# Performance work log

Hardware: AMD Instinct MI355X
Metric: run time of the kernel (lower is better)

## Reference

```python
import jax, jax.numpy as jnp
import numpy as np

N = 100000   # nodes
E = 3200000  # edges (avg degree 32)
G = 512      # graphs in batch
IN = 128     # in_channels
H1, C1 = 8, 8  # conv1 heads, per-head channels
OUT = 64     # out_channels (conv2, 1 head)
NEG_SLOPE = 0.2


def setup_inputs() -> dict:
    key = jax.random.key(0)
    ks = jax.random.split(key, 12)
    s = 0.1
    return dict(
        x=jax.random.normal(ks[0], (N, IN), jnp.float32),
        edge_index=jax.random.randint(ks[1], (2, E), 0, N),
        batch=jnp.sort(jax.random.randint(ks[2], (N,), 0, G)),
        W1=jax.random.normal(ks[3], (IN, H1 * C1), jnp.float32) * s,
        att_src1=jax.random.normal(ks[4], (H1, C1), jnp.float32) * s,
        att_dst1=jax.random.normal(ks[5], (H1, C1), jnp.float32) * s,
        b1=jnp.zeros((H1 * C1,), jnp.float32),
        W2=jax.random.normal(ks[6], (H1 * C1, OUT), jnp.float32) * s,
        att_src2=jax.random.normal(ks[7], (1, OUT), jnp.float32) * s,
        att_dst2=jax.random.normal(ks[8], (1, OUT), jnp.float32) * s,
        b2=jnp.zeros((OUT,), jnp.float32),
        lw1=jax.random.normal(ks[9], (OUT, 128), jnp.float32) * s,
        lb1=jnp.zeros((128,), jnp.float32),
        lw2=jax.random.normal(ks[10], (128, 1), jnp.float32) * s,
        lb2=jnp.zeros((1,), jnp.float32),
    )


def gat_layer(x, src, dst, W, a_src, a_dst, bias, heads, outc):
    # PyG GATConv (eval mode): linear -> per-edge leaky_relu attention ->
    # segment softmax over incoming edges per dst -> weighted scatter-add.
    n = x.shape[0]
    h = (x @ W).reshape(n, heads, outc)                      # [N,H,C]
    a_s = jnp.einsum('nhc,hc->nh', h, a_src)                 # [N,H]
    a_d = jnp.einsum('nhc,hc->nh', h, a_dst)
    e = jax.nn.leaky_relu(a_s[src] + a_d[dst], NEG_SLOPE)    # [E',H]
    m = jax.ops.segment_max(e, dst, num_segments=n)
    m = jax.lax.stop_gradient(jnp.where(jnp.isfinite(m), m, 0.0))
    ex = jnp.exp(e - m[dst])
    denom = jax.ops.segment_sum(ex, dst, num_segments=n)
    alpha = ex / jnp.maximum(denom[dst], 1e-16)              # [E',H]
    out = jax.ops.segment_sum(h[src] * alpha[:, :, None], dst, num_segments=n)
    return out.reshape(n, heads * outc) + bias


def reference(x, W1, att_src1, att_dst1, b1, W2, att_src2, att_dst2, b2,
              lw1, lb1, lw2, lb2, edge_index, batch):
    n = x.shape[0]
    loops = jnp.arange(n)                                    # add_self_loops=True
    src = jnp.concatenate([edge_index[0], loops])
    dst = jnp.concatenate([edge_index[1], loops])
    h = jax.nn.elu(gat_layer(x, src, dst, W1, att_src1, att_dst1, b1, H1, C1))
    h = gat_layer(h, src, dst, W2, att_src2, att_dst2, b2, 1, OUT)  # [N,OUT]
    # global_mean_pool
    s = jax.ops.segment_sum(h, batch, num_segments=G)
    cnt = jax.ops.segment_sum(jnp.ones((n, 1), h.dtype), batch, num_segments=G)
    g = s / jnp.maximum(cnt, 1.0)                            # [G,OUT]
    g = jax.nn.elu(g @ lw1 + lb1)
    return g @ lw2 + lb2                                     # [G,1]
```

## Files before the change

### kernel.cpp

```cpp
#include <hip/hip_runtime.h>
#include <hip/hip_fp16.h>
#include <math.h>

#define NN   100000
#define EE   3200000
#define GG   512
#define INC  128
#define D1   64
#define OUTC 64
#define HID  128
#define NEG  0.2f

#define BINS 391
#define BCAP 9216
#define BKBLK 1563
#define NGB 391

typedef __attribute__((ext_vector_type(2))) float v2f;

__global__ __launch_bounds__(256, 3)
void k_fused(const int* __restrict__ srcv, const int* __restrict__ dstv,
             int* __restrict__ cursor, int* __restrict__ bucket,
             const float* __restrict__ x, const float* __restrict__ W1,
             const float* __restrict__ att_s, const float* __restrict__ att_d,
             unsigned int* __restrict__ h1, __half* __restrict__ a_s,
             float* __restrict__ a_d) {
    __shared__ __align__(16) char smem[49152];
    int tid = threadIdx.x;
    if (blockIdx.x < NGB) {
        float4* sW4 = (float4*)smem;
        float (*sxT)[256] = (float(*)[256])(smem + 32768);
        const float4* W4 = (const float4*)W1;
        for (int i = tid; i < 128 * 16; i += 256) sW4[i] = W4[i];
        int node0 = blockIdx.x * 256;
        int rg = tid >> 3, cg = tid & 7;
        float acc[8][8];
#pragma unroll
        for (int ii = 0; ii < 8; ++ii)
#pragma unroll
            for (int jj = 0; jj < 8; ++jj) acc[ii][jj] = 0.f;
        const float4* x4 = (const float4*)x;
        for (int kt = 0; kt < 8; ++kt) {
            if (kt) __syncthreads();
#pragma unroll
            for (int q = 0; q < 4; ++q) {
                int i = q * 256 + tid;
                int r = i >> 2, kc = i & 3;
                int gn = node0 + r;
                float4 v = {0.f, 0.f, 0.f, 0.f};
                if (gn < NN) v = x4[(size_t)gn * 32 + kt * 4 + kc];
                int cs = r ^ (kc << 3);
                sxT[kc * 4 + 0][cs] = v.x;
                sxT[kc * 4 + 1][cs] = v.y;
                sxT[kc * 4 + 2][cs] = v.z;
                sxT[kc * 4 + 3][cs] = v.w;
            }
            __syncthreads();
#pragma unroll 4
            for (int kk = 0; kk < 16; ++kk) {
                int sw = (kk >> 2) << 3;
                const float* xr = &sxT[kk][(rg * 8) ^ sw];
                float4 xa = *(const float4*)xr;
                float4 xb = *(const float4*)(xr + 4);
                int kg = kt * 16 + kk;
                float4 wa = sW4[kg * 16 + cg * 2];
                float4 wb = sW4[kg * 16 + cg * 2 + 1];
                float xv[8] = {xa.x, xa.y, xa.z, xa.w, xb.x, xb.y, xb.z, xb.w};
                float wv[8] = {wa.x, wa.y, wa.z, wa.w, wb.x, wb.y, wb.z, wb.w};
#pragma unroll
                for (int ii = 0; ii < 8; ++ii)
#pragma unroll
                    for (int jj = 0; jj < 8; ++jj)
                        acc[ii][jj] = fmaf(xv[ii], wv[jj], acc[ii][jj]);
            }
        }
        float4 s0 = ((const float4*)att_s)[cg * 2];
        float4 s1 = ((const float4*)att_s)[cg * 2 + 1];
        float4 d0 = ((const float4*)att_d)[cg * 2];
        float4 d1 = ((const float4*)att_d)[cg * 2 + 1];
        uint2* hp2 = (uint2*)h1;
#pragma unroll
        for (int ii = 0; ii < 8; ++ii) {
            int n = node0 + rg * 8 + ii;
            if (n < NN) {
                float* a = acc[ii];
                int p0 = __builtin_amdgcn_cvt_pk_fp8_f32(a[0], a[1], 0, false);
                p0 = __builtin_amdgcn_cvt_pk_fp8_f32(a[2], a[3], p0, true);
                int p1 = __builtin_amdgcn_cvt_pk_fp8_f32(a[4], a[5], 0, false);
                p1 = __builtin_amdgcn_cvt_pk_fp8_f32(a[6], a[7], p1, true);
                uint2 pk; pk.x = (unsigned)p0; pk.y = (unsigned)p1;
                hp2[n * 8 + cg] = pk;
                float as = a[0] * s0.x;
                as = fmaf(a[1], s0.y, as); as = fmaf(a[2], s0.z, as);
                as = fmaf(a[3], s0.w, as); as = fmaf(a[4], s1.x, as);
                as = fmaf(a[5], s1.y, as); as = fmaf(a[6], s1.z, as);
                as = fmaf(a[7], s1.w, as);
                float ad = a[0] * d0.x;
                ad = fmaf(a[1], d0.y, ad); ad = fmaf(a[2], d0.z, ad);
                ad = fmaf(a[3], d0.w, ad); ad = fmaf(a[4], d1.x, ad);
                ad = fmaf(a[5], d1.y, ad); ad = fmaf(a[6], d1.z, ad);
                ad = fmaf(a[7], d1.w, ad);
                a_s[n * 8 + cg] = __float2half(as);
                a_d[n * 8 + cg] = ad;
            }
        }
    } else {
        int* hcnt  = (int*)smem;
        int* hbase = hcnt + BINS;
        for (int i = tid; i < BINS; i += 256) hcnt[i] = 0;
        __syncthreads();
        int e0 = (blockIdx.x - NGB) * 2048;
        int bn[8], rk[8], pk[8];
#pragma unroll
        for (int q = 0; q < 8; ++q) {
            int e = e0 + q * 256 + tid;
            if (e < EE) {
                int s = srcv[e], d = dstv[e];
                bn[q] = d >> 8;
                pk[q] = (s << 8) | (d & 255);
                rk[q] = atomicAdd(&hcnt[bn[q]], 1);
            } else bn[q] = -1;
        }
        __syncthreads();
        for (int i = tid; i < BINS; i += 256) {
            int c = hcnt[i];
            hbase[i] = c ? atomicAdd(&cursor[i], c) : 0;
        }
        __syncthreads();
#pragma unroll
        for (int q = 0; q < 8; ++q) {
            if (bn[q] >= 0) {
                int p = hbase[bn[q]] + rk[q];
                if (p < BCAP) bucket[bn[q] * BCAP + p] = pk[q];
            }
        }
    }
}

__global__ __launch_bounds__(256)
void k_binCSR(const int* __restrict__ cursor, const int* __restrict__ bucket,
              int* __restrict__ col, int* __restrict__ rbeg, int* __restrict__ rend) {
    __shared__ int cnt[256];
    __shared__ int tmp[256];
    __shared__ int cur[256];
    int b = blockIdx.x, tid = threadIdx.x;
    cnt[tid] = 0;
    __syncthreads();
    int m = cursor[b]; if (m > BCAP) m = BCAP;
    const int* seg = bucket + b * BCAP;
    for (int i = tid; i < m; i += 256)
        atomicAdd(&cnt[seg[i] & 255], 1);
    __syncthreads();
    tmp[tid] = cnt[tid];
    __syncthreads();
    for (int off = 1; off < 256; off <<= 1) {
        int t = (tid >= off) ? tmp[tid - off] : 0;
        __syncthreads();
        tmp[tid] += t;
        __syncthreads();
    }
    int excl = tmp[tid] - cnt[tid];
    int n = b * 256 + tid;
    if (n < NN) {
        rbeg[n] = b * BCAP + excl;
        rend[n] = b * BCAP + excl + cnt[tid];
    }
    cur[tid] = excl;
    __syncthreads();
    for (int i = tid; i < m; i += 256) {
        int pkv = seg[i];
        int r = atomicAdd(&cur[pkv & 255], 1);
        col[b * BCAP + r] = pkv >> 8;
    }
}

__global__ __launch_bounds__(256, 8)
void k_gat_agg1(const int* __restrict__ rbeg, const int* __restrict__ rend,
                const int* __restrict__ col,
                const __half* __restrict__ a_s, const float* __restrict__ a_d,
                const unsigned int* __restrict__ h1, const float* __restrict__ b1,
                float* __restrict__ out) {
    int wv = threadIdx.x >> 6;
    int lane = threadIdx.x & 63;
    int half = lane >> 5;
    int d = blockIdx.x * 8 + wv * 2 + half;
    int gs = (lane >> 3) & 3;
    int l = lane & 7;
    int rb = rbeg[d], re = rend[d];
    float adh = a_d[d * 8 + l];
    const uint2* hp = (const uint2*)h1;
    uint2 rself = hp[d * 8 + l];
    float asself = __half2float(a_s[d * 8 + l]);
    float ac[8] = {0.f,0.f,0.f,0.f,0.f,0.f,0.f,0.f};
    float denom = 0.f;
    int e = rb + gs;
    int s[4];
#pragma unroll
    for (int q = 0; q < 4; ++q) s[q] = col[e + 4 * q];
    for (; e + 12 < re; ) {
        uint2 rr[4]; float asv[4]; int sn[4];
#pragma unroll
        for (int q = 0; q < 4; ++q) rr[q] = hp[s[q] * 8 + l];
#pragma unroll
        for (int q = 0; q < 4; ++q) asv[q] = __half2float(a_s[s[q] * 8 + l]);
        int en = e + 16;
#pragma unroll
        for (int q = 0; q < 4; ++q) sn[q] = col[en + 4 * q];
#pragma unroll
        for (int q = 0; q < 4; ++q) {
            float xx = asv[q] + adh;
            xx = xx >= 0.f ? xx : NEG * xx;
            float w = __expf(xx);
            denom += w;
            v2f f0 = __builtin_amdgcn_cvt_pk_f32_fp8((int)rr[q].x, false);
            v2f f1 = __builtin_amdgcn_cvt_pk_f32_fp8((int)rr[q].x, true);
            v2f f2 = __builtin_amdgcn_cvt_pk_f32_fp8((int)rr[q].y, false);
            v2f f3 = __builtin_amdgcn_cvt_pk_f32_fp8((int)rr[q].y, true);
            ac[0] = fmaf(f0.x, w, ac[0]); ac[1] = fmaf(f0.y, w, ac[1]);
            ac[2] = fmaf(f1.x, w, ac[2]); ac[3] = fmaf(f1.y, w, ac[3]);
            ac[4] = fmaf(f2.x, w, ac[4]); ac[5] = fmaf(f2.y, w, ac[5]);
            ac[6] = fmaf(f3.x, w, ac[6]); ac[7] = fmaf(f3.y, w, ac[7]);
        }
        e = en;
#pragma unroll
        for (int q = 0; q < 4; ++q) s[q] = sn[q];
    }
    for (; e < re; e += 4) {
        int s0 = col[e];
        uint2 r0 = hp[s0 * 8 + l];
        float x0 = __half2float(a_s[s0 * 8 + l]) + adh;
        x0 = x0 >= 0.f ? x0 : NEG * x0;
        float w0 = __expf(x0);
        denom += w0;
        v2f f0 = __builtin_amdgcn_cvt_pk_f32_fp8((int)r0.x, false);
        v2f f1 = __builtin_amdgcn_cvt_pk_f32_fp8((int)r0.x, true);
        v2f f2 = __builtin_amdgcn_cvt_pk_f32_fp8((int)r0.y, false);
        v2f f3 = __builtin_amdgcn_cvt_pk_f32_fp8((int)r0.y, true);
        ac[0] = fmaf(f0.x, w0, ac[0]); ac[1] = fmaf(f0.y, w0, ac[1]);
        ac[2] = fmaf(f1.x, w0, ac[2]); ac[3] = fmaf(f1.y, w0, ac[3]);
        ac[4] = fmaf(f2.x, w0, ac[4]); ac[5] = fmaf(f2.y, w0, ac[5]);
        ac[6] = fmaf(f3.x, w0, ac[6]); ac[7] = fmaf(f3.y, w0, ac[7]);
    }
    if (gs == 0) {
        float es = asself + adh;
        es = es >= 0.f ? es : NEG * es;
        float w = __expf(es);
        denom += w;
        v2f f0 = __builtin_amdgcn_cvt_pk_f32_fp8((int)rself.x, false);
        v2f f1 = __builtin_amdgcn_cvt_pk_f32_fp8((int)rself.x, true);
        v2f f2 = __builtin_amdgcn_cvt_pk_f32_fp8((int)rself.y, false);
        v2f f3 = __builtin_amdgcn_cvt_pk_f32_fp8((int)rself.y, true);
        ac[0] = fmaf(f0.x, w, ac[0]); ac[1] = fmaf(f0.y, w, ac[1]);
        ac[2] = fmaf(f1.x, w, ac[2]); ac[3] = fmaf(f1.y, w, ac[3]);
        ac[4] = fmaf(f2.x, w, ac[4]); ac[5] = fmaf(f2.y, w, ac[5]);
        ac[6] = fmaf(f3.x, w, ac[6]); ac[7] = fmaf(f3.y, w, ac[7]);
    }
#pragma unroll
    for (int i = 0; i < 8; ++i) {
        ac[i] += __shfl_xor(ac[i], 8, 64);
        ac[i] += __shfl_xor(ac[i], 16, 64);
    }
    denom += __shfl_xor(denom, 8, 64);
    denom += __shfl_xor(denom, 16, 64);
    if (gs == 0) {
        float inv = 1.0f / denom;
        float4 b0 = ((const float4*)b1)[l * 2];
        float4 b4 = ((const float4*)b1)[l * 2 + 1];
        float4 r0, r1;
        r0.x = fmaf(ac[0], inv, b0.x); r0.x = r0.x > 0.f ? r0.x : expm1f(r0.x);
        r0.y = fmaf(ac[1], inv, b0.y); r0.y = r0.y > 0.f ? r0.y : expm1f(r0.y);
        r0.z = fmaf(ac[2], inv, b0.z); r0.z = r0.z > 0.f ? r0.z : expm1f(r0.z);
        r0.w = fmaf(ac[3], inv, b0.w); r0.w = r0.w > 0.f ? r0.w : expm1f(r0.w);
        r1.x = fmaf(ac[4], inv, b4.x); r1.x = r1.x > 0.f ? r1.x : expm1f(r1.x);
        r1.y = fmaf(ac[5], inv, b4.y); r1.y = r1.y > 0.f ? r1.y : expm1f(r1.y);
        r1.z = fmaf(ac[6], inv, b4.z); r1.z = r1.z > 0.f ? r1.z : expm1f(r1.z);
        r1.w = fmaf(ac[7], inv, b4.w); r1.w = r1.w > 0.f ? r1.w : expm1f(r1.w);
        ((float4*)out)[d * 16 + l * 2]     = r0;
        ((float4*)out)[d * 16 + l * 2 + 1] = r1;
    }
}

__global__ __launch_bounds__(256, 3)
void k_lin2(const float* __restrict__ hin, const float* __restrict__ W2,
            const float* __restrict__ att_s, const float* __restrict__ att_d,
            unsigned int* __restrict__ h2, float* __restrict__ a_s,
            float* __restrict__ a_d) {
    __shared__ float4 sW4[D1 * 16];
    __shared__ float sxT[32][256];
    int tid = threadIdx.x;
    const float4* W4 = (const float4*)W2;
    for (int i = tid; i < D1 * 16; i += 256) sW4[i] = W4[i];
    int node0 = blockIdx.x * 256;
    int rg = tid >> 3, cg = tid & 7;
    float acc[8][8];
#pragma unroll
    for (int ii = 0; ii < 8; ++ii)
#pragma unroll
        for (int jj = 0; jj < 8; ++jj) acc[ii][jj] = 0.f;
    const float4* x4 = (const float4*)hin;
    for (int kt = 0; kt < 2; ++kt) {
        if (kt) __syncthreads();
#pragma unroll
        for (int q = 0; q < 8; ++q) {
            int i = q * 256 + tid;
            int r = i >> 3, kc = i & 7;
            int gn = node0 + r;
            float4 v = {0.f, 0.f, 0.f, 0.f};
            if (gn < NN) v = x4[(size_t)gn * 16 + kt * 8 + kc];
            int cs = r ^ (kc << 3);
            sxT[kc * 4 + 0][cs] = v.x;
            sxT[kc * 4 + 1][cs] = v.y;
            sxT[kc * 4 + 2][cs] = v.z;
            sxT[kc * 4 + 3][cs] = v.w;
        }
        __syncthreads();
#pragma unroll 4
        for (int kk = 0; kk < 32; ++kk) {
            int sw = (kk >> 2) << 3;
            const float* xr = &sxT[kk][(rg * 8) ^ sw];
            float4 xa = *(const float4*)xr;
            float4 xb = *(const float4*)(xr + 4);
            int kg = kt * 32 + kk;
            float4 wa = sW4[kg * 16 + cg * 2];
            float4 wb = sW4[kg * 16 + cg * 2 + 1];
            float xv[8] = {xa.x, xa.y, xa.z, xa.w, xb.x, xb.y, xb.z, xb.w};
            float wv[8] = {wa.x, wa.y, wa.z, wa.w, wb.x, wb.y, wb.z, wb.w};
#pragma unroll
            for (int ii = 0; ii < 8; ++ii)
#pragma unroll
                for (int jj = 0; jj < 8; ++jj)
                    acc[ii][jj] = fmaf(xv[ii], wv[jj], acc[ii][jj]);
        }
    }
    float4 s0 = ((const float4*)att_s)[cg * 2];
    float4 s1 = ((const float4*)att_s)[cg * 2 + 1];
    float4 d0 = ((const float4*)att_d)[cg * 2];
    float4 d1 = ((const float4*)att_d)[cg * 2 + 1];
    uint2* hp2 = (uint2*)h2;
#pragma unroll
    for (int ii = 0; ii < 8; ++ii) {
        int n = node0 + rg * 8 + ii;
        if (n < NN) {
            float* a = acc[ii];
            int p0 = __builtin_amdgcn_cvt_pk_fp8_f32(a[0], a[1], 0, false);
            p0 = __builtin_amdgcn_cvt_pk_fp8_f32(a[2], a[3], p0, true);
            int p1 = __builtin_amdgcn_cvt_pk_fp8_f32(a[4], a[5], 0, false);
            p1 = __builtin_amdgcn_cvt_pk_fp8_f32(a[6], a[7], p1, true);
            uint2 pk; pk.x = (unsigned)p0; pk.y = (unsigned)p1;
            hp2[n * 8 + cg] = pk;
            float vs = a[0] * s0.x;
            vs = fmaf(a[1], s0.y, vs); vs = fmaf(a[2], s0.z, vs);
            vs = fmaf(a[3], s0.w, vs); vs = fmaf(a[4], s1.x, vs);
            vs = fmaf(a[5], s1.y, vs); vs = fmaf(a[6], s1.z, vs);
            vs = fmaf(a[7], s1.w, vs);
            float vd = a[0] * d0.x;
            vd = fmaf(a[1], d0.y, vd); vd = fmaf(a[2], d0.z, vd);
            vd = fmaf(a[3], d0.w, vd); vd = fmaf(a[4], d1.x, vd);
            vd = fmaf(a[5], d1.y, vd); vd = fmaf(a[6], d1.z, vd);
            vd = fmaf(a[7], d1.w, vd);
            vs += __shfl_xor(vs, 1, 64); vs += __shfl_xor(vs, 2, 64);
            vs += __shfl_xor(vs, 4, 64);
            vd += __shfl_xor(vd, 1, 64); vd += __shfl_xor(vd, 2, 64);
            vd += __shfl_xor(vd, 4, 64);
            if (cg == 0) { a_s[n] = vs; a_d[n] = vd; }
        }
    }
}

__global__ __launch_bounds__(256, 8)
void k_gat_agg2(const int* __restrict__ rbeg, const int* __restrict__ rend,
                const int* __restrict__ col,
                const float* __restrict__ a_s, const float* __restrict__ a_d,
                const unsigned int* __restrict__ h2, const float* __restrict__ b2,
                const int* __restrict__ batch,
                float* __restrict__ pool, float* __restrict__ cnt) {
    __shared__ float sv[8][64];
    __shared__ int sgi[8];
    int wv = threadIdx.x >> 6;
    int lane = threadIdx.x & 63;
    int half = lane >> 5;
    int idx = wv * 2 + half;
    int d = blockIdx.x * 8 + idx;
    int gs = (lane >> 3) & 3;
    int l = lane & 7;
    int rb = rbeg[d], re = rend[d];
    float ad = a_d[d];
    const uint2* hp = (const uint2*)h2;
    uint2 rself = hp[d * 8 + l];
    float asself = a_s[d];
    if (gs == 0 && l == 0) sgi[idx] = batch[d];
    float ac[8] = {0.f,0.f,0.f,0.f,0.f,0.f,0.f,0.f};
    float denom = 0.f;
    int e = rb + gs;
    int s[4];
#pragma unroll
    for (int q = 0; q < 4; ++q) s[q] = col[e + 4 * q];
    for (; e + 12 < re; ) {
        uint2 rr[4]; float asv[4]; int sn[4];
#pragma unroll
        for (int q = 0; q < 4; ++q) rr[q] = hp[s[q] * 8 + l];
#pragma unroll
        for (int q = 0; q < 4; ++q) asv[q] = a_s[s[q]];
        int en = e + 16;
#pragma unroll
        for (int q = 0; q < 4; ++q) sn[q] = col[en + 4 * q];
#pragma unroll
        for (int q = 0; q < 4; ++q) {
            float xx = asv[q] + ad;
            xx = xx >= 0.f ? xx : NEG * xx;
            float w = __expf(xx);
            denom += w;
            v2f f0 = __builtin_amdgcn_cvt_pk_f32_fp8((int)rr[q].x, false);
            v2f f1 = __builtin_amdgcn_cvt_pk_f32_fp8((int)rr[q].x, true);
            v2f f2 = __builtin_amdgcn_cvt_pk_f32_fp8((int)rr[q].y, false);
            v2f f3 = __builtin_amdgcn_cvt_pk_f32_fp8((int)rr[q].y, true);
            ac[0] = fmaf(f0.x, w, ac[0]); ac[1] = fmaf(f0.y, w, ac[1]);
            ac[2] = fmaf(f1.x, w, ac[2]); ac[3] = fmaf(f1.y, w, ac[3]);
            ac[4] = fmaf(f2.x, w, ac[4]); ac[5] = fmaf(f2.y, w, ac[5]);
            ac[6] = fmaf(f3.x, w, ac[6]); ac[7] = fmaf(f3.y, w, ac[7]);
        }
        e = en;
#pragma unroll
        for (int q = 0; q < 4; ++q) s[q] = sn[q];
    }
    for (; e < re; e += 4) {
        int s0 = col[e];
        uint2 r0 = hp[s0 * 8 + l];
        float x0 = a_s[s0] + ad;
        x0 = x0 >= 0.f ? x0 : NEG * x0;
        float w0 = __expf(x0);
        denom += w0;
        v2f f0 = __builtin_amdgcn_cvt_pk_f32_fp8((int)r0.x, false);
        v2f f1 = __builtin_amdgcn_cvt_pk_f32_fp8((int)r0.x, true);
        v2f f2 = __builtin_amdgcn_cvt_pk_f32_fp8((int)r0.y, false);
        v2f f3 = __builtin_amdgcn_cvt_pk_f32_fp8((int)r0.y, true);
        ac[0] = fmaf(f0.x, w0, ac[0]); ac[1] = fmaf(f0.y, w0, ac[1]);
        ac[2] = fmaf(f1.x, w0, ac[2]); ac[3] = fmaf(f1.y, w0, ac[3]);
        ac[4] = fmaf(f2.x, w0, ac[4]); ac[5] = fmaf(f2.y, w0, ac[5]);
        ac[6] = fmaf(f3.x, w0, ac[6]); ac[7] = fmaf(f3.y, w0, ac[7]);
    }
    if (gs == 0) {
        float es = asself + ad;
        es = es >= 0.f ? es : NEG * es;
        float w = __expf(es);
        denom += w;
        v2f f0 = __builtin_amdgcn_cvt_pk_f32_fp8((int)rself.x, false);
        v2f f1 = __builtin_amdgcn_cvt_pk_f32_fp8((int)rself.x, true);
        v2f f2 = __builtin_amdgcn_cvt_pk_f32_fp8((int)rself.y, false);
        v2f f3 = __builtin_amdgcn_cvt_pk_f32_fp8((int)rself.y, true);
        ac[0] = fmaf(f0.x, w, ac[0]); ac[1] = fmaf(f0.y, w, ac[1]);
        ac[2] = fmaf(f1.x, w, ac[2]); ac[3] = fmaf(f1.y, w, ac[3]);
        ac[4] = fmaf(f2.x, w, ac[4]); ac[5] = fmaf(f2.y, w, ac[5]);
        ac[6] = fmaf(f3.x, w, ac[6]); ac[7] = fmaf(f3.y, w, ac[7]);
    }
#pragma unroll
    for (int i = 0; i < 8; ++i) {
        ac[i] += __shfl_xor(ac[i], 8, 64);
        ac[i] += __shfl_xor(ac[i], 16, 64);
    }
    denom += __shfl_xor(denom, 8, 64);
    denom += __shfl_xor(denom, 16, 64);
    if (gs == 0) {
        float inv = 1.0f / denom;
#pragma unroll
        for (int i = 0; i < 8; ++i)
            sv[idx][l * 8 + i] = fmaf(ac[i], inv, b2[l * 8 + i]);
    }
    __syncthreads();
    int tid = threadIdx.x;
    if (tid < 64) {
        float acc = sv[0][tid]; int curg = sgi[0];
        for (int r = 1; r < 8; ++r) {
            if (sgi[r] == curg) acc += sv[r][tid];
            else { atomicAdd(&pool[curg * 64 + tid], acc); curg = sgi[r]; acc = sv[r][tid]; }
        }
        atomicAdd(&pool[curg * 64 + tid], acc);
    } else if (tid == 64) {
        float c = 1.f; int curg = sgi[0];
        for (int r = 1; r < 8; ++r) {
            if (sgi[r] == curg) c += 1.f;
            else { atomicAdd(&cnt[curg], c); curg = sgi[r]; c = 1.f; }
        }
        atomicAdd(&cnt[curg], c);
    }
}

__global__ __launch_bounds__(128)
void k_mlp(const float* __restrict__ pool, const float* __restrict__ cnt,
           const float* __restrict__ lw1, const float* __restrict__ lb1,
           const float* __restrict__ lw2, const float* __restrict__ lb2,
           float* __restrict__ out) {
    __shared__ float sg[OUTC];
    __shared__ float sh[HID];
    int g = blockIdx.x, tid = threadIdx.x;
    float c = fmaxf(cnt[g], 1.0f);
    if (tid < OUTC) sg[tid] = pool[g * OUTC + tid] / c;
    __syncthreads();
    float acc = lb1[tid];
#pragma unroll 8
    for (int k = 0; k < OUTC; ++k)
        acc = fmaf(sg[k], lw1[k * HID + tid], acc);
    acc = acc > 0.f ? acc : expm1f(acc);
    sh[tid] = acc * lw2[tid];
    __syncthreads();
    for (int off = 64; off >= 1; off >>= 1) {
        if (tid < off) sh[tid] += sh[tid + off];
        __syncthreads();
    }
    if (tid == 0) out[g] = sh[0] + lb2[0];
}

extern "C" void kernel_launch(void* const* d_in, const int* in_sizes, int n_in,
                              void* d_out, int out_size, void* d_ws, size_t ws_size,
                              hipStream_t stream) {
    const float* x    = (const float*)d_in[0];
    const int*   ei   = (const int*)d_in[1];
    const int*   batch= (const int*)d_in[2];
    const float* W1   = (const float*)d_in[3];
    const float* as1  = (const float*)d_in[4];
    const float* ad1  = (const float*)d_in[5];
    const float* b1   = (const float*)d_in[6];
    const float* W2   = (const float*)d_in[7];
    const float* as2  = (const float*)d_in[8];
    const float* ad2  = (const float*)d_in[9];
    const float* b2   = (const float*)d_in[10];
    const float* lw1  = (const float*)d_in[11];
    const float* lb1  = (const float*)d_in[12];
    const float* lw2  = (const float*)d_in[13];
    const float* lb2  = (const float*)d_in[14];
    float* out = (float*)d_out;

    unsigned int* H8 = (unsigned int*)d_ws;
    float* B    = (float*)(H8 + (size_t)NN * 16);
    float* aD1  = B + (size_t)NN * 64;
    float* aS2  = aD1 + NN * 8;
    float* aD2  = aS2 + NN;
    float* pool = aD2 + NN;
    float* cnt  = pool + GG * 64;
    __half* aS1h = (__half*)(cnt + GG);
    int* rbeg   = (int*)(aS1h + (size_t)NN * 8);
    int* rend   = rbeg + NN;
    int* cursor = rend + NN;
    int* bucket = cursor + BINS;
    int* colv   = bucket + (size_t)BINS * BCAP;

    const int* srcv = ei;
    const int* dstv = ei + EE;

    hipMemsetAsync(cursor, 0, BINS * sizeof(int), stream);
    hipMemsetAsync(pool, 0, (size_t)(GG * 64 + GG) * sizeof(float), stream);

    k_fused<<<NGB + BKBLK, 256, 0, stream>>>(srcv, dstv, cursor, bucket,
                                             x, W1, as1, ad1, H8, aS1h, aD1);
    k_binCSR<<<BINS, 256, 0, stream>>>(cursor, bucket, colv, rbeg, rend);

    k_gat_agg1<<<NN / 8, 256, 0, stream>>>(rbeg, rend, colv, aS1h, aD1, H8, b1, B);

    k_lin2    <<<NGB, 256, 0, stream>>>(B, W2, as2, ad2, H8, aS2, aD2);
    k_gat_agg2<<<NN / 8, 256, 0, stream>>>(rbeg, rend, colv, aS2, aD2, H8, b2, batch, pool, cnt);

    k_mlp<<<GG, 128, 0, stream>>>(pool, cnt, lw1, lb1, lw2, lb2, out);
}
```

Before: 353.2 us.

## Split fp8 feature table into two column slabs and aggregate in two passes

Stores the fp8 node features as two separate half-width slabs (32 channels each) and runs each GAT aggregation kernel twice, once per slab. Each pass gathers only 4 bytes per lane, so a pass's working set of gathered rows is half as large and fits better in cache. The cost is reading the CSR column list, recomputing the attention exponentials twice, and extra launches. Column-index loads and layer-1 output stores are also made nontemporal.

```diff
diff --git a/kernel.cpp b/kernel.cpp
--- a/kernel.cpp
+++ b/kernel.cpp
@@ -17,6 +17,7 @@
 #define NGB 391
 
 typedef __attribute__((ext_vector_type(2))) float v2f;
+typedef __attribute__((ext_vector_type(4))) float v4f;
 
 __global__ __launch_bounds__(256, 3)
 void k_fused(const int* __restrict__ srcv, const int* __restrict__ dstv,
@@ -78,7 +79,8 @@
         float4 s1 = ((const float4*)att_s)[cg * 2 + 1];
         float4 d0 = ((const float4*)att_d)[cg * 2];
         float4 d1 = ((const float4*)att_d)[cg * 2 + 1];
-        uint2* hp2 = (uint2*)h1;
+        uint2* slab2 = (uint2*)(h1 + (size_t)(cg >> 2) * NN * 8);
+        int cj = cg & 3;
 #pragma unroll
         for (int ii = 0; ii < 8; ++ii) {
             int n = node0 + rg * 8 + ii;
@@ -89,7 +91,7 @@
                 int p1 = __builtin_amdgcn_cvt_pk_fp8_f32(a[4], a[5], 0, false);
                 p1 = __builtin_amdgcn_cvt_pk_fp8_f32(a[6], a[7], p1, true);
                 uint2 pk; pk.x = (unsigned)p0; pk.y = (unsigned)p1;
-                hp2[n * 8 + cg] = pk;
+                slab2[n * 4 + cj] = pk;
                 float as = a[0] * s0.x;
                 as = fmaf(a[1], s0.y, as); as = fmaf(a[2], s0.z, as);
                 as = fmaf(a[3], s0.w, as); as = fmaf(a[4], s1.x, as);
@@ -174,6 +176,7 @@
     }
 }
 
+template<int PASS>
 __global__ __launch_bounds__(256, 8)
 void k_gat_agg1(const int* __restrict__ rbeg, const int* __restrict__ rend,
                 const int* __restrict__ col,
@@ -186,77 +189,66 @@
     int d = blockIdx.x * 8 + wv * 2 + half;
     int gs = (lane >> 3) & 3;
     int l = lane & 7;
+    int hd = PASS * 4 + (l >> 1);
+    const unsigned int* hp = h1 + (size_t)PASS * NN * 8;
     int rb = rbeg[d], re = rend[d];
-    float adh = a_d[d * 8 + l];
-    const uint2* hp = (const uint2*)h1;
-    uint2 rself = hp[d * 8 + l];
-    float asself = __half2float(a_s[d * 8 + l]);
-    float ac[8] = {0.f,0.f,0.f,0.f,0.f,0.f,0.f,0.f};
+    float adh = a_d[d * 8 + hd];
+    unsigned int rself = hp[d * 8 + l];
+    float asself = __half2float(a_s[d * 8 + hd]);
+    float ac[4] = {0.f, 0.f, 0.f, 0.f};
     float denom = 0.f;
     int e = rb + gs;
     int s[4];
 #pragma unroll
-    for (int q = 0; q < 4; ++q) s[q] = col[e + 4 * q];
+    for (int q = 0; q < 4; ++q) s[q] = __builtin_nontemporal_load(col + e + 4 * q);
     for (; e + 12 < re; ) {
-        uint2 rr[4]; float asv[4]; int sn[4];
+        unsigned int rr[4]; float asv[4]; int sn[4];
 #pragma unroll
         for (int q = 0; q < 4; ++q) rr[q] = hp[s[q] * 8 + l];
 #pragma unroll
-        for (int q = 0; q < 4; ++q) asv[q] = __half2float(a_s[s[q] * 8 + l]);
+        for (int q = 0; q < 4; ++q) asv[q] = __half2float(a_s[s[q] * 8 + hd]);
         int en = e + 16;
 #pragma unroll
-        for (int q = 0; q < 4; ++q) sn[q] = col[en + 4 * q];
+        for (int q = 0; q < 4; ++q) sn[q] = __builtin_nontemporal_load(col + en + 4 * q);
 #pragma unroll
         for (int q = 0; q < 4; ++q) {
             float xx = asv[q] + adh;
             xx = xx >= 0.f ? xx : NEG * xx;
             float w = __expf(xx);
             denom += w;
-            v2f f0 = __builtin_amdgcn_cvt_pk_f32_fp8((int)rr[q].x, false);
-            v2f f1 = __builtin_amdgcn_cvt_pk_f32_fp8((int)rr[q].x, true);
-            v2f f2 = __builtin_amdgcn_cvt_pk_f32_fp8((int)rr[q].y, false);
-            v2f f3 = __builtin_amdgcn_cvt_pk_f32_fp8((int)rr[q].y, true);
+            v2f f0 = __builtin_amdgcn_cvt_pk_f32_fp8((int)rr[q], false);
+            v2f f1 = __builtin_amdgcn_cvt_pk_f32_fp8((int)rr[q], true);
             ac[0] = fmaf(f0.x, w, ac[0]); ac[1] = fmaf(f0.y, w, ac[1]);
             ac[2] = fmaf(f1.x, w, ac[2]); ac[3] = fmaf(f1.y, w, ac[3]);
-            ac[4] = fmaf(f2.x, w, ac[4]); ac[5] = fmaf(f2.y, w, ac[5]);
-            ac[6] = fmaf(f3.x, w, ac[6]); ac[7] = fmaf(f3.y, w, ac[7]);
         }
         e = en;
 #pragma unroll
         for (int q = 0; q < 4; ++q) s[q] = sn[q];
     }
     for (; e < re; e += 4) {
-        int s0 = col[e];
-        uint2 r0 = hp[s0 * 8 + l];
-        float x0 = __half2float(a_s[s0 * 8 + l]) + adh;
+        int s0 = __builtin_nontemporal_load(col + e);
+        unsigned int r0 = hp[s0 * 8 + l];
+        float x0 = __half2float(a_s[s0 * 8 + hd]) + adh;
         x0 = x0 >= 0.f ? x0 : NEG * x0;
         float w0 = __expf(x0);
         denom += w0;
-        v2f f0 = __builtin_amdgcn_cvt_pk_f32_fp8((int)r0.x, false);
-        v2f f1 = __builtin_amdgcn_cvt_pk_f32_fp8((int)r0.x, true);
-        v2f f2 = __builtin_amdgcn_cvt_pk_f32_fp8((int)r0.y, false);
-        v2f f3 = __builtin_amdgcn_cvt_pk_f32_fp8((int)r0.y, true);
+        v2f f0 = __builtin_amdgcn_cvt_pk_f32_fp8((int)r0, false);
+        v2f f1 = __builtin_amdgcn_cvt_pk_f32_fp8((int)r0, true);
         ac[0] = fmaf(f0.x, w0, ac[0]); ac[1] = fmaf(f0.y, w0, ac[1]);
         ac[2] = fmaf(f1.x, w0, ac[2]); ac[3] = fmaf(f1.y, w0, ac[3]);
-        ac[4] = fmaf(f2.x, w0, ac[4]); ac[5] = fmaf(f2.y, w0, ac[5]);
-        ac[6] = fmaf(f3.x, w0, ac[6]); ac[7] = fmaf(f3.y, w0, ac[7]);
     }
     if (gs == 0) {
         float es = asself + adh;
         es = es >= 0.f ? es : NEG * es;
         float w = __expf(es);
         denom += w;
-        v2f f0 = __builtin_amdgcn_cvt_pk_f32_fp8((int)rself.x, false);
-        v2f f1 = __builtin_amdgcn_cvt_pk_f32_fp8((int)rself.x, true);
-        v2f f2 = __builtin_amdgcn_cvt_pk_f32_fp8((int)rself.y, false);
-        v2f f3 = __builtin_amdgcn_cvt_pk_f32_fp8((int)rself.y, true);
+        v2f f0 = __builtin_amdgcn_cvt_pk_f32_fp8((int)rself, false);
+        v2f f1 = __builtin_amdgcn_cvt_pk_f32_fp8((int)rself, true);
         ac[0] = fmaf(f0.x, w, ac[0]); ac[1] = fmaf(f0.y, w, ac[1]);
         ac[2] = fmaf(f1.x, w, ac[2]); ac[3] = fmaf(f1.y, w, ac[3]);
-        ac[4] = fmaf(f2.x, w, ac[4]); ac[5] = fmaf(f2.y, w, ac[5]);
-        ac[6] = fmaf(f3.x, w, ac[6]); ac[7] = fmaf(f3.y, w, ac[7]);
-    }
-#pragma unroll
-    for (int i = 0; i < 8; ++i) {
+    }
+#pragma unroll
+    for (int i = 0; i < 4; ++i) {
         ac[i] += __shfl_xor(ac[i], 8, 64);
         ac[i] += __shfl_xor(ac[i], 16, 64);
     }
@@ -264,19 +256,13 @@
     denom += __shfl_xor(denom, 16, 64);
     if (gs == 0) {
         float inv = 1.0f / denom;
-        float4 b0 = ((const float4*)b1)[l * 2];
-        float4 b4 = ((const float4*)b1)[l * 2 + 1];
-        float4 r0, r1;
+        float4 b0 = ((const float4*)b1)[PASS * 8 + l];
+        v4f r0;
         r0.x = fmaf(ac[0], inv, b0.x); r0.x = r0.x > 0.f ? r0.x : expm1f(r0.x);
         r0.y = fmaf(ac[1], inv, b0.y); r0.y = r0.y > 0.f ? r0.y : expm1f(r0.y);
         r0.z = fmaf(ac[2], inv, b0.z); r0.z = r0.z > 0.f ? r0.z : expm1f(r0.z);
         r0.w = fmaf(ac[3], inv, b0.w); r0.w = r0.w > 0.f ? r0.w : expm1f(r0.w);
-        r1.x = fmaf(ac[4], inv, b4.x); r1.x = r1.x > 0.f ? r1.x : expm1f(r1.x);
-        r1.y = fmaf(ac[5], inv, b4.y); r1.y = r1.y > 0.f ? r1.y : expm1f(r1.y);
-        r1.z = fmaf(ac[6], inv, b4.z); r1.z = r1.z > 0.f ? r1.z : expm1f(r1.z);
-        r1.w = fmaf(ac[7], inv, b4.w); r1.w = r1.w > 0.f ? r1.w : expm1f(r1.w);
-        ((float4*)out)[d * 16 + l * 2]     = r0;
-        ((float4*)out)[d * 16 + l * 2 + 1] = r1;
+        __builtin_nontemporal_store(r0, (v4f*)out + d * 16 + PASS * 8 + l);
     }
 }
 
@@ -336,7 +322,8 @@
     float4 s1 = ((const float4*)att_s)[cg * 2 + 1];
     float4 d0 = ((const float4*)att_d)[cg * 2];
     float4 d1 = ((const float4*)att_d)[cg * 2 + 1];
-    uint2* hp2 = (uint2*)h2;
+    uint2* slab2 = (uint2*)(h2 + (size_t)(cg >> 2) * NN * 8);
+    int cj = cg & 3;
 #pragma unroll
     for (int ii = 0; ii < 8; ++ii) {
         int n = node0 + rg * 8 + ii;
@@ -347,7 +334,7 @@
             int p1 = __builtin_amdgcn_cvt_pk_fp8_f32(a[4], a[5], 0, false);
             p1 = __builtin_amdgcn_cvt_pk_fp8_f32(a[6], a[7], p1, true);
             uint2 pk; pk.x = (unsigned)p0; pk.y = (unsigned)p1;
-            hp2[n * 8 + cg] = pk;
+            slab2[n * 4 + cj] = pk;
             float vs = a[0] * s0.x;
             vs = fmaf(a[1], s0.y, vs); vs = fmaf(a[2], s0.z, vs);
             vs = fmaf(a[3], s0.w, vs); vs = fmaf(a[4], s1.x, vs);
@@ -367,6 +354,7 @@
     }
 }
 
+template<int PASS>
 __global__ __launch_bounds__(256, 8)
 void k_gat_agg2(const int* __restrict__ rbeg, const int* __restrict__ rend,
                 const int* __restrict__ col,
@@ -374,7 +362,7 @@
                 const unsigned int* __restrict__ h2, const float* __restrict__ b2,
                 const int* __restrict__ batch,
                 float* __restrict__ pool, float* __restrict__ cnt) {
-    __shared__ float sv[8][64];
+    __shared__ float sv[8][32];
     __shared__ int sgi[8];
     int wv = threadIdx.x >> 6;
     int lane = threadIdx.x & 63;
@@ -383,78 +371,66 @@
     int d = blockIdx.x * 8 + idx;
     int gs = (lane >> 3) & 3;
     int l = lane & 7;
+    const unsigned int* hp = h2 + (size_t)PASS * NN * 8;
     int rb = rbeg[d], re = rend[d];
     float ad = a_d[d];
-    const uint2* hp = (const uint2*)h2;
-    uint2 rself = hp[d * 8 + l];
+    unsigned int rself = hp[d * 8 + l];
     float asself = a_s[d];
     if (gs == 0 && l == 0) sgi[idx] = batch[d];
-    float ac[8] = {0.f,0.f,0.f,0.f,0.f,0.f,0.f,0.f};
+    float ac[4] = {0.f, 0.f, 0.f, 0.f};
     float denom = 0.f;
     int e = rb + gs;
     int s[4];
 #pragma unroll
-    for (int q = 0; q < 4; ++q) s[q] = col[e + 4 * q];
+    for (int q = 0; q < 4; ++q) s[q] = __builtin_nontemporal_load(col + e + 4 * q);
     for (; e + 12 < re; ) {
-        uint2 rr[4]; float asv[4]; int sn[4];
+        unsigned int rr[4]; float asv[4]; int sn[4];
 #pragma unroll
         for (int q = 0; q < 4; ++q) rr[q] = hp[s[q] * 8 + l];
 #pragma unroll
         for (int q = 0; q < 4; ++q) asv[q] = a_s[s[q]];
         int en = e + 16;
 #pragma unroll
-        for (int q = 0; q < 4; ++q) sn[q] = col[en + 4 * q];
+        for (int q = 0; q < 4; ++q) sn[q] = __builtin_nontemporal_load(col + en + 4 * q);
 #pragma unroll
         for (int q = 0; q < 4; ++q) {
             float xx = asv[q] + ad;
             xx = xx >= 0.f ? xx : NEG * xx;
             float w = __expf(xx);
             denom += w;
-            v2f f0 = __builtin_amdgcn_cvt_pk_f32_fp8((int)rr[q].x, false);
-            v2f f1 = __builtin_amdgcn_cvt_pk_f32_fp8((int)rr[q].x, true);
-            v2f f2 = __builtin_amdgcn_cvt_pk_f32_fp8((int)rr[q].y, false);
-            v2f f3 = __builtin_amdgcn_cvt_pk_f32_fp8((int)rr[q].y, true);
+            v2f f0 = __builtin_amdgcn_cvt_pk_f32_fp8((int)rr[q], false);
+            v2f f1 = __builtin_amdgcn_cvt_pk_f32_fp8((int)rr[q], true);
             ac[0] = fmaf(f0.x, w, ac[0]); ac[1] = fmaf(f0.y, w, ac[1]);
             ac[2] = fmaf(f1.x, w, ac[2]); ac[3] = fmaf(f1.y, w, ac[3]);
-            ac[4] = fmaf(f2.x, w, ac[4]); ac[5] = fmaf(f2.y, w, ac[5]);
-            ac[6] = fmaf(f3.x, w, ac[6]); ac[7] = fmaf(f3.y, w, ac[7]);
         }
         e = en;
 #pragma unroll
         for (int q = 0; q < 4; ++q) s[q] = sn[q];
     }
     for (; e < re; e += 4) {
-        int s0 = col[e];
-        uint2 r0 = hp[s0 * 8 + l];
+        int s0 = __builtin_nontemporal_load(col + e);
+        unsigned int r0 = hp[s0 * 8 + l];
         float x0 = a_s[s0] + ad;
         x0 = x0 >= 0.f ? x0 : NEG * x0;
         float w0 = __expf(x0);
         denom += w0;
-        v2f f0 = __builtin_amdgcn_cvt_pk_f32_fp8((int)r0.x, false);
-        v2f f1 = __builtin_amdgcn_cvt_pk_f32_fp8((int)r0.x, true);
-        v2f f2 = __builtin_amdgcn_cvt_pk_f32_fp8((int)r0.y, false);
-        v2f f3 = __builtin_amdgcn_cvt_pk_f32_fp8((int)r0.y, true);
+        v2f f0 = __builtin_amdgcn_cvt_pk_f32_fp8((int)r0, false);
+        v2f f1 = __builtin_amdgcn_cvt_pk_f32_fp8((int)r0, true);
         ac[0] = fmaf(f0.x, w0, ac[0]); ac[1] = fmaf(f0.y, w0, ac[1]);
         ac[2] = fmaf(f1.x, w0, ac[2]); ac[3] = fmaf(f1.y, w0, ac[3]);
-        ac[4] = fmaf(f2.x, w0, ac[4]); ac[5] = fmaf(f2.y, w0, ac[5]);
-        ac[6] = fmaf(f3.x, w0, ac[6]); ac[7] = fmaf(f3.y, w0, ac[7]);
     }
     if (gs == 0) {
         float es = asself + ad;
         es = es >= 0.f ? es : NEG * es;
         float w = __expf(es);
         denom += w;
-        v2f f0 = __builtin_amdgcn_cvt_pk_f32_fp8((int)rself.x, false);
-        v2f f1 = __builtin_amdgcn_cvt_pk_f32_fp8((int)rself.x, true);
-        v2f f2 = __builtin_amdgcn_cvt_pk_f32_fp8((int)rself.y, false);
-        v2f f3 = __builtin_amdgcn_cvt_pk_f32_fp8((int)rself.y, true);
+        v2f f0 = __builtin_amdgcn_cvt_pk_f32_fp8((int)rself, false);
+        v2f f1 = __builtin_amdgcn_cvt_pk_f32_fp8((int)rself, true);
         ac[0] = fmaf(f0.x, w, ac[0]); ac[1] = fmaf(f0.y, w, ac[1]);
         ac[2] = fmaf(f1.x, w, ac[2]); ac[3] = fmaf(f1.y, w, ac[3]);
-        ac[4] = fmaf(f2.x, w, ac[4]); ac[5] = fmaf(f2.y, w, ac[5]);
-        ac[6] = fmaf(f3.x, w, ac[6]); ac[7] = fmaf(f3.y, w, ac[7]);
-    }
-#pragma unroll
-    for (int i = 0; i < 8; ++i) {
+    }
+#pragma unroll
+    for (int i = 0; i < 4; ++i) {
         ac[i] += __shfl_xor(ac[i], 8, 64);
         ac[i] += __shfl_xor(ac[i], 16, 64);
     }
@@ -463,19 +439,19 @@
     if (gs == 0) {
         float inv = 1.0f / denom;
 #pragma unroll
-        for (int i = 0; i < 8; ++i)
-            sv[idx][l * 8 + i] = fmaf(ac[i], inv, b2[l * 8 + i]);
+        for (int i = 0; i < 4; ++i)
+            sv[idx][l * 4 + i] = fmaf(ac[i], inv, b2[PASS * 32 + l * 4 + i]);
     }
     __syncthreads();
     int tid = threadIdx.x;
-    if (tid < 64) {
+    if (tid < 32) {
         float acc = sv[0][tid]; int curg = sgi[0];
         for (int r = 1; r < 8; ++r) {
             if (sgi[r] == curg) acc += sv[r][tid];
-            else { atomicAdd(&pool[curg * 64 + tid], acc); curg = sgi[r]; acc = sv[r][tid]; }
-        }
-        atomicAdd(&pool[curg * 64 + tid], acc);
-    } else if (tid == 64) {
+            else { atomicAdd(&pool[curg * 64 + PASS * 32 + tid], acc); curg = sgi[r]; acc = sv[r][tid]; }
+        }
+        atomicAdd(&pool[curg * 64 + PASS * 32 + tid], acc);
+    } else if (PASS == 0 && tid == 32) {
         float c = 1.f; int curg = sgi[0];
         for (int r = 1; r < 8; ++r) {
             if (sgi[r] == curg) c += 1.f;
@@ -554,10 +530,12 @@
                                              x, W1, as1, ad1, H8, aS1h, aD1);
     k_binCSR<<<BINS, 256, 0, stream>>>(cursor, bucket, colv, rbeg, rend);
 
-    k_gat_agg1<<<NN / 8, 256, 0, stream>>>(rbeg, rend, colv, aS1h, aD1, H8, b1, B);
-
-    k_lin2    <<<NGB, 256, 0, stream>>>(B, W2, as2, ad2, H8, aS2, aD2);
-    k_gat_agg2<<<NN / 8, 256, 0, stream>>>(rbeg, rend, colv, aS2, aD2, H8, b2, batch, pool, cnt);
+    k_gat_agg1<0><<<NN / 8, 256, 0, stream>>>(rbeg, rend, colv, aS1h, aD1, H8, b1, B);
+    k_gat_agg1<1><<<NN / 8, 256, 0, stream>>>(rbeg, rend, colv, aS1h, aD1, H8, b1, B);
+
+    k_lin2<<<NGB, 256, 0, stream>>>(B, W2, as2, ad2, H8, aS2, aD2);
+    k_gat_agg2<0><<<NN / 8, 256, 0, stream>>>(rbeg, rend, colv, aS2, aD2, H8, b2, batch, pool, cnt);
+    k_gat_agg2<1><<<NN / 8, 256, 0, stream>>>(rbeg, rend, colv, aS2, aD2, H8, b2, batch, pool, cnt);
 
     k_mlp<<<GG, 128, 0, stream>>>(pool, cnt, lw1, lb1, lw2, lb2, out);
 }
```

New measurement: 469.6 us. 1.33x slower.

## Interleave fp8 features and source attention into 128-byte node records; halve bucket width

Applied to the files above, without the earlier changes.

Each node now has one 128-byte record holding its fp8 features (64 bytes) followed by its source-attention logits, fp16 for layer 1 and fp32 for layer 2. A gathered neighbor's features and logit therefore come from the same cache line instead of two separate arrays. Destination binning also changes from 256 to 128 nodes per bin, which doubles the bin count and lowers per-bin capacity to 4800. The records double the workspace footprint, and the smaller capacity increases the risk of overflow truncation for high in-degree bins.

```diff
diff --git a/kernel.cpp b/kernel.cpp
--- a/kernel.cpp
+++ b/kernel.cpp
@@ -11,20 +11,23 @@
 #define HID  128
 #define NEG  0.2f
 
-#define BINS 391
-#define BCAP 9216
+#define BINS   782
+#define BNODE  128
+#define BSHIFT 7
+#define BMASK  127
+#define BCAP   4800
 #define BKBLK 1563
 #define NGB 391
 
 typedef __attribute__((ext_vector_type(2))) float v2f;
+
 
 __global__ __launch_bounds__(256, 3)
 void k_fused(const int* __restrict__ srcv, const int* __restrict__ dstv,
              int* __restrict__ cursor, int* __restrict__ bucket,
              const float* __restrict__ x, const float* __restrict__ W1,
              const float* __restrict__ att_s, const float* __restrict__ att_d,
-             unsigned int* __restrict__ h1, __half* __restrict__ a_s,
-             float* __restrict__ a_d) {
+             unsigned int* __restrict__ rec, float* __restrict__ a_d) {
     __shared__ __align__(16) char smem[49152];
     int tid = threadIdx.x;
     if (blockIdx.x < NGB) {
@@ -78,7 +81,8 @@
         float4 s1 = ((const float4*)att_s)[cg * 2 + 1];
         float4 d0 = ((const float4*)att_d)[cg * 2];
         float4 d1 = ((const float4*)att_d)[cg * 2 + 1];
-        uint2* hp2 = (uint2*)h1;
+        uint2* hp2 = (uint2*)rec;
+        __half* ash = (__half*)rec;
 #pragma unroll
         for (int ii = 0; ii < 8; ++ii) {
             int n = node0 + rg * 8 + ii;
@@ -89,7 +93,7 @@
                 int p1 = __builtin_amdgcn_cvt_pk_fp8_f32(a[4], a[5], 0, false);
                 p1 = __builtin_amdgcn_cvt_pk_fp8_f32(a[6], a[7], p1, true);
                 uint2 pk; pk.x = (unsigned)p0; pk.y = (unsigned)p1;
-                hp2[n * 8 + cg] = pk;
+                hp2[n * 16 + cg] = pk;
                 float as = a[0] * s0.x;
                 as = fmaf(a[1], s0.y, as); as = fmaf(a[2], s0.z, as);
                 as = fmaf(a[3], s0.w, as); as = fmaf(a[4], s1.x, as);
@@ -100,7 +104,7 @@
                 ad = fmaf(a[3], d0.w, ad); ad = fmaf(a[4], d1.x, ad);
                 ad = fmaf(a[5], d1.y, ad); ad = fmaf(a[6], d1.z, ad);
                 ad = fmaf(a[7], d1.w, ad);
-                a_s[n * 8 + cg] = __float2half(as);
+                ash[n * 64 + 32 + cg] = __float2half(as);
                 a_d[n * 8 + cg] = ad;
             }
         }
@@ -116,8 +120,8 @@
             int e = e0 + q * 256 + tid;
             if (e < EE) {
                 int s = srcv[e], d = dstv[e];
-                bn[q] = d >> 8;
-                pk[q] = (s << 8) | (d & 255);
+                bn[q] = d >> BSHIFT;
+                pk[q] = (s << BSHIFT) | (d & BMASK);
                 rk[q] = atomicAdd(&hcnt[bn[q]], 1);
             } else bn[q] = -1;
         }
@@ -140,46 +144,47 @@
 __global__ __launch_bounds__(256)
 void k_binCSR(const int* __restrict__ cursor, const int* __restrict__ bucket,
               int* __restrict__ col, int* __restrict__ rbeg, int* __restrict__ rend) {
-    __shared__ int cnt[256];
-    __shared__ int tmp[256];
-    __shared__ int cur[256];
+    __shared__ int cnt_[BNODE];
+    __shared__ int tmp[BNODE];
+    __shared__ int cur[BNODE];
     int b = blockIdx.x, tid = threadIdx.x;
-    cnt[tid] = 0;
+    if (tid < BNODE) cnt_[tid] = 0;
     __syncthreads();
     int m = cursor[b]; if (m > BCAP) m = BCAP;
     const int* seg = bucket + b * BCAP;
     for (int i = tid; i < m; i += 256)
-        atomicAdd(&cnt[seg[i] & 255], 1);
-    __syncthreads();
-    tmp[tid] = cnt[tid];
-    __syncthreads();
-    for (int off = 1; off < 256; off <<= 1) {
-        int t = (tid >= off) ? tmp[tid - off] : 0;
-        __syncthreads();
-        tmp[tid] += t;
-        __syncthreads();
-    }
-    int excl = tmp[tid] - cnt[tid];
-    int n = b * 256 + tid;
-    if (n < NN) {
-        rbeg[n] = b * BCAP + excl;
-        rend[n] = b * BCAP + excl + cnt[tid];
-    }
-    cur[tid] = excl;
+        atomicAdd(&cnt_[seg[i] & BMASK], 1);
+    __syncthreads();
+    if (tid < BNODE) tmp[tid] = cnt_[tid];
+    __syncthreads();
+    for (int off = 1; off < BNODE; off <<= 1) {
+        int t = (tid >= off && tid < BNODE) ? tmp[tid - off] : 0;
+        __syncthreads();
+        if (tid < BNODE) tmp[tid] += t;
+        __syncthreads();
+    }
+    if (tid < BNODE) {
+        int excl = tmp[tid] - cnt_[tid];
+        int n = b * BNODE + tid;
+        if (n < NN) {
+            rbeg[n] = b * BCAP + excl;
+            rend[n] = b * BCAP + excl + cnt_[tid];
+        }
+        cur[tid] = excl;
+    }
     __syncthreads();
     for (int i = tid; i < m; i += 256) {
         int pkv = seg[i];
-        int r = atomicAdd(&cur[pkv & 255], 1);
-        col[b * BCAP + r] = pkv >> 8;
+        int r = atomicAdd(&cur[pkv & BMASK], 1);
+        col[b * BCAP + r] = pkv >> BSHIFT;
     }
 }
 
 __global__ __launch_bounds__(256, 8)
 void k_gat_agg1(const int* __restrict__ rbeg, const int* __restrict__ rend,
                 const int* __restrict__ col,
-                const __half* __restrict__ a_s, const float* __restrict__ a_d,
-                const unsigned int* __restrict__ h1, const float* __restrict__ b1,
-                float* __restrict__ out) {
+                const unsigned int* __restrict__ rec, const float* __restrict__ a_d,
+                const float* __restrict__ b1, float* __restrict__ out) {
     int wv = threadIdx.x >> 6;
     int lane = threadIdx.x & 63;
     int half = lane >> 5;
@@ -188,9 +193,10 @@
     int l = lane & 7;
     int rb = rbeg[d], re = rend[d];
     float adh = a_d[d * 8 + l];
-    const uint2* hp = (const uint2*)h1;
-    uint2 rself = hp[d * 8 + l];
-    float asself = __half2float(a_s[d * 8 + l]);
+    const uint2* hp = (const uint2*)rec;
+    const __half* asr = (const __half*)rec;
+    uint2 rself = hp[d * 16 + l];
+    float asself = __half2float(asr[d * 64 + 32 + l]);
     float ac[8] = {0.f,0.f,0.f,0.f,0.f,0.f,0.f,0.f};
     float denom = 0.f;
     int e = rb + gs;
@@ -200,9 +206,9 @@
     for (; e + 12 < re; ) {
         uint2 rr[4]; float asv[4]; int sn[4];
 #pragma unroll
-        for (int q = 0; q < 4; ++q) rr[q] = hp[s[q] * 8 + l];
-#pragma unroll
-        for (int q = 0; q < 4; ++q) asv[q] = __half2float(a_s[s[q] * 8 + l]);
+        for (int q = 0; q < 4; ++q) rr[q] = hp[(unsigned)(s[q] * 16 + l)];
+#pragma unroll
+        for (int q = 0; q < 4; ++q) asv[q] = __half2float(asr[(unsigned)(s[q] * 64 + 32 + l)]);
         int en = e + 16;
 #pragma unroll
         for (int q = 0; q < 4; ++q) sn[q] = col[en + 4 * q];
@@ -227,8 +233,8 @@
     }
     for (; e < re; e += 4) {
         int s0 = col[e];
-        uint2 r0 = hp[s0 * 8 + l];
-        float x0 = __half2float(a_s[s0 * 8 + l]) + adh;
+        uint2 r0 = hp[(unsigned)(s0 * 16 + l)];
+        float x0 = __half2float(asr[(unsigned)(s0 * 64 + 32 + l)]) + adh;
         x0 = x0 >= 0.f ? x0 : NEG * x0;
         float w0 = __expf(x0);
         denom += w0;
@@ -283,8 +289,7 @@
 __global__ __launch_bounds__(256, 3)
 void k_lin2(const float* __restrict__ hin, const float* __restrict__ W2,
             const float* __restrict__ att_s, const float* __restrict__ att_d,
-            unsigned int* __restrict__ h2, float* __restrict__ a_s,
-            float* __restrict__ a_d) {
+            unsigned int* __restrict__ rec, float* __restrict__ a_d) {
     __shared__ float4 sW4[D1 * 16];
     __shared__ float sxT[32][256];
     int tid = threadIdx.x;
@@ -336,7 +341,7 @@
     float4 s1 = ((const float4*)att_s)[cg * 2 + 1];
     float4 d0 = ((const float4*)att_d)[cg * 2];
     float4 d1 = ((const float4*)att_d)[cg * 2 + 1];
-    uint2* hp2 = (uint2*)h2;
+    uint2* hp2 = (uint2*)rec;
 #pragma unroll
     for (int ii = 0; ii < 8; ++ii) {
         int n = node0 + rg * 8 + ii;
@@ -347,7 +352,7 @@
             int p1 = __builtin_amdgcn_cvt_pk_fp8_f32(a[4], a[5], 0, false);
             p1 = __builtin_amdgcn_cvt_pk_fp8_f32(a[6], a[7], p1, true);
             uint2 pk; pk.x = (unsigned)p0; pk.y = (unsigned)p1;
-            hp2[n * 8 + cg] = pk;
+            hp2[n * 16 + cg] = pk;
             float vs = a[0] * s0.x;
             vs = fmaf(a[1], s0.y, vs); vs = fmaf(a[2], s0.z, vs);
             vs = fmaf(a[3], s0.w, vs); vs = fmaf(a[4], s1.x, vs);
@@ -362,7 +367,10 @@
             vs += __shfl_xor(vs, 4, 64);
             vd += __shfl_xor(vd, 1, 64); vd += __shfl_xor(vd, 2, 64);
             vd += __shfl_xor(vd, 4, 64);
-            if (cg == 0) { a_s[n] = vs; a_d[n] = vd; }
+            if (cg == 0) {
+                ((float*)rec)[(size_t)n * 32 + 16] = vs;
+                a_d[n] = vd;
+            }
         }
     }
 }
@@ -370,9 +378,8 @@
 __global__ __launch_bounds__(256, 8)
 void k_gat_agg2(const int* __restrict__ rbeg, const int* __restrict__ rend,
                 const int* __restrict__ col,
-                const float* __restrict__ a_s, const float* __restrict__ a_d,
-                const unsigned int* __restrict__ h2, const float* __restrict__ b2,
-                const int* __restrict__ batch,
+                const unsigned int* __restrict__ rec, const float* __restrict__ a_d,
+                const float* __restrict__ b2, const int* __restrict__ batch,
                 float* __restrict__ pool, float* __restrict__ cnt) {
     __shared__ float sv[8][64];
     __shared__ int sgi[8];
@@ -385,9 +392,10 @@
     int l = lane & 7;
     int rb = rbeg[d], re = rend[d];
     float ad = a_d[d];
-    const uint2* hp = (const uint2*)h2;
-    uint2 rself = hp[d * 8 + l];
-    float asself = a_s[d];
+    const uint2* hp = (const uint2*)rec;
+    const float* recf = (const float*)rec;
+    uint2 rself = hp[d * 16 + l];
+    float asself = recf[d * 32 + 16];
     if (gs == 0 && l == 0) sgi[idx] = batch[d];
     float ac[8] = {0.f,0.f,0.f,0.f,0.f,0.f,0.f,0.f};
     float denom = 0.f;
@@ -398,9 +406,9 @@
     for (; e + 12 < re; ) {
         uint2 rr[4]; float asv[4]; int sn[4];
 #pragma unroll
-        for (int q = 0; q < 4; ++q) rr[q] = hp[s[q] * 8 + l];
-#pragma unroll
-        for (int q = 0; q < 4; ++q) asv[q] = a_s[s[q]];
+        for (int q = 0; q < 4; ++q) rr[q] = hp[(unsigned)(s[q] * 16 + l)];
+#pragma unroll
+        for (int q = 0; q < 4; ++q) asv[q] = recf[(unsigned)(s[q] * 32 + 16)];
         int en = e + 16;
 #pragma unroll
         for (int q = 0; q < 4; ++q) sn[q] = col[en + 4 * q];
@@ -425,8 +433,8 @@
     }
     for (; e < re; e += 4) {
         int s0 = col[e];
-        uint2 r0 = hp[s0 * 8 + l];
-        float x0 = a_s[s0] + ad;
+        uint2 r0 = hp[(unsigned)(s0 * 16 + l)];
+        float x0 = recf[(unsigned)(s0 * 32 + 16)] + ad;
         x0 = x0 >= 0.f ? x0 : NEG * x0;
         float w0 = __expf(x0);
         denom += w0;
@@ -530,15 +538,13 @@
     const float* lb2  = (const float*)d_in[14];
     float* out = (float*)d_out;
 
-    unsigned int* H8 = (unsigned int*)d_ws;
-    float* B    = (float*)(H8 + (size_t)NN * 16);
+    unsigned int* REC = (unsigned int*)d_ws;
+    float* B    = (float*)(REC + (size_t)NN * 32);
     float* aD1  = B + (size_t)NN * 64;
-    float* aS2  = aD1 + NN * 8;
-    float* aD2  = aS2 + NN;
+    float* aD2  = aD1 + (size_t)NN * 8;
     float* pool = aD2 + NN;
     float* cnt  = pool + GG * 64;
-    __half* aS1h = (__half*)(cnt + GG);
-    int* rbeg   = (int*)(aS1h + (size_t)NN * 8);
+    int* rbeg   = (int*)(cnt + GG);
     int* rend   = rbeg + NN;
     int* cursor = rend + NN;
     int* bucket = cursor + BINS;
@@ -551,13 +557,13 @@
     hipMemsetAsync(pool, 0, (size_t)(GG * 64 + GG) * sizeof(float), stream);
 
     k_fused<<<NGB + BKBLK, 256, 0, stream>>>(srcv, dstv, cursor, bucket,
-                                             x, W1, as1, ad1, H8, aS1h, aD1);
+                                             x, W1, as1, ad1, REC, aD1);
     k_binCSR<<<BINS, 256, 0, stream>>>(cursor, bucket, colv, rbeg, rend);
 
-    k_gat_agg1<<<NN / 8, 256, 0, stream>>>(rbeg, rend, colv, aS1h, aD1, H8, b1, B);
-
-    k_lin2    <<<NGB, 256, 0, stream>>>(B, W2, as2, ad2, H8, aS2, aD2);
-    k_gat_agg2<<<NN / 8, 256, 0, stream>>>(rbeg, rend, colv, aS2, aD2, H8, b2, batch, pool, cnt);
+    k_gat_agg1<<<NN / 8, 256, 0, stream>>>(rbeg, rend, colv, REC, aD1, b1, B);
+
+    k_lin2    <<<NGB, 256, 0, stream>>>(B, W2, as2, ad2, REC, aD2);
+    k_gat_agg2<<<NN / 8, 256, 0, stream>>>(rbeg, rend, colv, REC, aD2, b2, batch, pool, cnt);
 
     k_mlp<<<GG, 128, 0, stream>>>(pool, cnt, lw1, lb1, lw2, lb2, out);
 }
```

Measured after the change: 350.8 us. Within noise of the previous version (-0.7%).
